# Optimization experiments

Hardware: AMD Instinct MI355X
Metric: run time of the kernel (lower is better)

Reference implementation:

```python
import jax, jax.numpy as jnp
import numpy as np

HUGE = 1e8  # stand-in for ops.HUGE_INT

B, P, Q, PD, QD = 16, 1024, 512, 768, 768


def setup_inputs() -> dict:
    key = jax.random.key(0)
    k1, k2, k3, k4, k5 = jax.random.split(key, 5)
    p = jax.random.normal(k1, (B, P, PD), dtype=jnp.float32)
    q = jax.random.normal(k2, (B, Q, QD), dtype=jnp.float32)
    # True = padded position (masked out before softmax)
    p_masks = jax.random.randint(k3, (B, P), 0, 2).astype(bool)
    q_masks = jax.random.randint(k4, (B, Q), 0, 2).astype(bool)
    # projection weight of Linear(q_dim, p_dim, bias=False): [p_dim, q_dim]
    W = jax.random.normal(k5, (PD, QD), dtype=jnp.float32) / np.sqrt(QD)
    return {"p": p, "q": q, "p_masks": p_masks, "q_masks": q_masks, "W": W}


def reference(p, q, p_masks, q_masks, W):
    # q_proj = project(q): [B,Q,p_dim]; dropout=0.0 -> identity
    q_proj = jnp.einsum('bqd,pd->bqp', q, W)
    # affinity = p @ q_proj^T : [B,P,Q]
    affinity = jnp.einsum('bpd,bqd->bpq', p, q_proj)
    # normalize over dim 1 with padding mask broadcast over last dim
    attn_over_p = jax.nn.softmax(
        jnp.where(p_masks[:, :, None], -HUGE, affinity), axis=1)  # [B,P,Q]
    attn_over_q = jax.nn.softmax(
        jnp.where(q_masks[:, :, None], -HUGE, jnp.swapaxes(affinity, 1, 2)), axis=1)  # [B,Q,P]
    # attn(weights[B,W2,W3], cand[B,W2,C3]) -> [B,W3,C3] = weights^T @ cand
    q_to_p_attn_vec = jnp.einsum('bpq,bpd->bqd', attn_over_p, p)  # [B,Q,p_dim]
    cand = jnp.concatenate([q, q_to_p_attn_vec], axis=2)  # [B,Q,q_dim+p_dim]
    p_to_q_attn_vec = jnp.einsum('bqp,bqc->bpc', attn_over_q, cand)  # [B,P,q_dim+p_dim]
    return (p_to_q_attn_vec, q_to_p_attn_vec)
```

## Files before the change

kernel.cpp:

```cpp
#include <hip/hip_runtime.h>
#include <math.h>

constexpr int B_  = 16;
constexpr int P_  = 1024;
constexpr int Q_  = 512;
constexpr int PD_ = 768;
constexpr int QD_ = 768;
constexpr int CD_ = 1536;

#define HUGE_NEG (-1e8f)

typedef __attribute__((ext_vector_type(8))) _Float16 f16x8;
typedef __attribute__((ext_vector_type(4))) _Float16 f16x4;
typedef __attribute__((ext_vector_type(4))) float f32x4;

__device__ __forceinline__ void dma16(const void* g, void* l) {
  __builtin_amdgcn_global_load_lds((__attribute__((address_space(1))) void*)g,
                                   (__attribute__((address_space(3))) void*)l,
                                   16, 0, 0);
}

__global__ __launch_bounds__(256) void k_cvt(const float* __restrict__ src,
                                             _Float16* __restrict__ dst, int n8) {
  int i = blockIdx.x * 256 + threadIdx.x;
  if (i >= n8) return;
  float4 a = ((const float4*)src)[2 * i];
  float4 b = ((const float4*)src)[2 * i + 1];
  f16x8 o = {(_Float16)a.x, (_Float16)a.y, (_Float16)a.z, (_Float16)a.w,
             (_Float16)b.x, (_Float16)b.y, (_Float16)b.z, (_Float16)b.w};
  ((f16x8*)dst)[i] = o;
}

__global__ __launch_bounds__(256) void k_t2b16(const float* __restrict__ src,
                                               _Float16* __restrict__ dst,
                                               int R, int C, size_t dstBatch,
                                               int colOff) {
  __shared__ _Float16 T[64][72];
  int r0 = blockIdx.x * 64, c0 = blockIdx.y * 64, b = blockIdx.z;
  const float* S = src + (size_t)b * R * C;
  int tid = threadIdx.x;
  int rr = tid >> 4;
  int cc = (tid & 15) * 4;
#pragma unroll
  for (int k = 0; k < 4; ++k) {
    int r = rr + k * 16;
    float4 v = *(const float4*)(S + (size_t)(r0 + r) * C + c0 + cc);
    T[cc + 0][r] = (_Float16)v.x;
    T[cc + 1][r] = (_Float16)v.y;
    T[cc + 2][r] = (_Float16)v.z;
    T[cc + 3][r] = (_Float16)v.w;
  }
  __syncthreads();
  int cr = tid >> 2;
  int rc = (tid & 3) * 16;
  _Float16* D = dst + (size_t)b * dstBatch + (size_t)(colOff + c0 + cr) * R + r0;
  *(f16x8*)(D + rc) = *(f16x8*)&T[cr][rc];
  *(f16x8*)(D + rc + 8) = *(f16x8*)&T[cr][rc + 8];
}

__global__ __launch_bounds__(256) void k_rowWP(const float* __restrict__ aff,
                                               const int* __restrict__ qmask,
                                               _Float16* __restrict__ WP) {
  int row = blockIdx.x * 4 + (threadIdx.x >> 6);
  int lane = threadIdx.x & 63;
  int b = row >> 10;
  const float* r = aff + (size_t)row * Q_;
  const int* qm = qmask + b * Q_;
  int q0 = lane * 4;
  float4 x = *(const float4*)(r + q0);
  float4 y = *(const float4*)(r + q0 + 256);
  int4 ma = *(const int4*)(qm + q0);
  int4 mb = *(const int4*)(qm + q0 + 256);
  float v[8];
  v[0] = ma.x ? HUGE_NEG : x.x;
  v[1] = ma.y ? HUGE_NEG : x.y;
  v[2] = ma.z ? HUGE_NEG : x.z;
  v[3] = ma.w ? HUGE_NEG : x.w;
  v[4] = mb.x ? HUGE_NEG : y.x;
  v[5] = mb.y ? HUGE_NEG : y.y;
  v[6] = mb.z ? HUGE_NEG : y.z;
  v[7] = mb.w ? HUGE_NEG : y.w;
  float m = v[0];
#pragma unroll
  for (int j = 1; j < 8; ++j) m = fmaxf(m, v[j]);
#pragma unroll
  for (int off = 32; off > 0; off >>= 1) m = fmaxf(m, __shfl_xor(m, off));
  float s = 0.f;
#pragma unroll
  for (int j = 0; j < 8; ++j) s += __expf(v[j] - m);
#pragma unroll
  for (int off = 32; off > 0; off >>= 1) s += __shfl_xor(s, off);
  float inv = 1.0f / s;
  f16x4 w0, w1;
#pragma unroll
  for (int j = 0; j < 4; ++j) {
    w0[j] = (_Float16)(__expf(v[j] - m) * inv);
    w1[j] = (_Float16)(__expf(v[j + 4] - m) * inv);
  }
  _Float16* D = WP + (size_t)row * Q_;
  *(f16x4*)(D + q0) = w0;
  *(f16x4*)(D + q0 + 256) = w1;
}

__global__ __launch_bounds__(256) void k_colmerge(
    const float* __restrict__ pmax_part, const float* __restrict__ psum_part,
    float* __restrict__ colmax, float* __restrict__ colsum) {
  int b = blockIdx.x;
  int q = blockIdx.y * 256 + threadIdx.x;
  float m = -INFINITY;
#pragma unroll
  for (int z = 0; z < 8; ++z) m = fmaxf(m, pmax_part[(b * 8 + z) * Q_ + q]);
  float s = 0.f;
#pragma unroll
  for (int z = 0; z < 8; ++z)
    s += psum_part[(b * 8 + z) * Q_ + q] *
         __expf(pmax_part[(b * 8 + z) * Q_ + q] - m);
  colmax[b * Q_ + q] = m;
  colsum[b * Q_ + q] = s;
}

__global__ __launch_bounds__(256) void k_wq16(const float* __restrict__ aff,
                                              const int* __restrict__ pmask,
                                              const float* __restrict__ colmax,
                                              const float* __restrict__ colsum,
                                              _Float16* __restrict__ WQ) {
  __shared__ _Float16 T[64][72];
  __shared__ float cmx[64], cinv[64];
  int p0 = blockIdx.x * 64, q0 = blockIdx.y * 64, b = blockIdx.z;
  int tid = threadIdx.x;
  if (tid < 64) {
    cmx[tid] = colmax[b * Q_ + q0 + tid];
    cinv[tid] = 1.0f / colsum[b * Q_ + q0 + tid];
  }
  __syncthreads();
  const float* A = aff + (size_t)b * P_ * Q_;
  const int* pm = pmask + b * P_;
  int rr = tid >> 4;
  int cc = (tid & 15) * 4;
#pragma unroll
  for (int k = 0; k < 4; ++k) {
    int r = rr + k * 16;
    int msk = pm[p0 + r];
    float4 v = *(const float4*)(A + (size_t)(p0 + r) * Q_ + q0 + cc);
    float vv[4] = {v.x, v.y, v.z, v.w};
#pragma unroll
    for (int j = 0; j < 4; ++j) {
      float e = __expf((msk ? HUGE_NEG : vv[j]) - cmx[cc + j]) * cinv[cc + j];
      T[cc + j][r] = (_Float16)e;
    }
  }
  __syncthreads();
  int cr = tid >> 2;
  int rc = (tid & 3) * 16;
  _Float16* D = WQ + ((size_t)b * Q_ + q0 + cr) * P_ + p0;
  *(f16x8*)(D + rc) = *(f16x8*)&T[cr][rc];
  *(f16x8*)(D + rc + 8) = *(f16x8*)&T[cr][rc + 8];
}

template <int NT, int LDA, int LDB>
__device__ __forceinline__ void gemm_core(const _Float16* __restrict__ Ab,
                                          const _Float16* __restrict__ Bb,
                                          _Float16* As, _Float16* Bs,
                                          f32x4 (&acc)[4][4], int w, int l) {
  constexpr int TSZ = 128 * 32;
  int rA = w * 32 + (l >> 2);
  int sA = ((l & 3) ^ ((rA >> 1) & 3)) * 8;
  int fr = l & 15;
  int fsw = (((l >> 4) ^ ((fr >> 1) & 3))) * 8;
  int wr = w >> 1, wc = w & 1;

  auto stage = [&](int buf, int t) {
    const _Float16* ga = Ab + (size_t)rA * LDA + t * 32 + sA;
    const _Float16* gb = Bb + (size_t)rA * LDB + t * 32 + sA;
    _Float16* la = As + buf * TSZ + (w * 32) * 32;
    _Float16* lb = Bs + buf * TSZ + (w * 32) * 32;
    dma16(ga, la);
    dma16(ga + 16 * LDA, la + 16 * 32);
    dma16(gb, lb);
    dma16(gb + 16 * LDB, lb + 16 * 32);
  };
  auto compute = [&](int buf) {
    const _Float16* A0 = As + buf * TSZ;
    const _Float16* B0 = Bs + buf * TSZ;
    f16x8 a[4];
#pragma unroll
    for (int m = 0; m < 4; ++m)
      a[m] = *(const f16x8*)(A0 + (wr * 64 + m * 16 + fr) * 32 + fsw);
#pragma unroll
    for (int n = 0; n < 4; ++n) {
      f16x8 bn = *(const f16x8*)(B0 + (wc * 64 + n * 16 + fr) * 32 + fsw);
#pragma unroll
      for (int m = 0; m < 4; ++m)
        acc[m][n] =
            __builtin_amdgcn_mfma_f32_16x16x32_f16(a[m], bn, acc[m][n], 0, 0, 0);
    }
  };

  stage(0, 0);
  stage(1, 1);
  int b0 = 0, b1 = 1, b2 = 2;
#pragma unroll 3
  for (int t = 0; t < NT - 2; ++t) {
    stage(b2, t + 2);
    asm volatile("s_waitcnt vmcnt(8)" ::: "memory");
    __builtin_amdgcn_s_barrier();
    __builtin_amdgcn_sched_barrier(0);
    compute(b0);
    __builtin_amdgcn_s_barrier();
    int tmp = b0; b0 = b1; b1 = b2; b2 = tmp;
  }
  asm volatile("s_waitcnt vmcnt(4)" ::: "memory");
  __builtin_amdgcn_s_barrier();
  __builtin_amdgcn_sched_barrier(0);
  compute(b0);
  __builtin_amdgcn_s_barrier();
  asm volatile("s_waitcnt vmcnt(0)" ::: "memory");
  __builtin_amdgcn_s_barrier();
  __builtin_amdgcn_sched_barrier(0);
  compute(b1);
}

#define SWZ_DECODE(GX, GY)                                          \
  int lin = blockIdx.x + (GX) * (blockIdx.y + (GY) * blockIdx.z);   \
  constexpr int NWG = (GX) * (GY) * B_;                             \
  int w8 = (lin & 7) * (NWG / 8) + (lin >> 3);                      \
  int j0 = (w8 % (GX)) * 128;                                      \
  int t_ = w8 / (GX);                                               \
  int i0 = (t_ % (GY)) * 128;                                       \
  int b = t_ / (GY);

__global__ __launch_bounds__(256) void k1_proj(const _Float16* __restrict__ q16,
                                               const _Float16* __restrict__ W16,
                                               _Float16* __restrict__ qp) {
  __shared__ alignas(16) _Float16 As[3 * 128 * 32];
  __shared__ alignas(16) _Float16 Bs[3 * 128 * 32];
  SWZ_DECODE(PD_ / 128, Q_ / 128)
  int tid = threadIdx.x, w = tid >> 6, l = tid & 63;
  f32x4 acc[4][4];
#pragma unroll
  for (int m = 0; m < 4; ++m)
#pragma unroll
    for (int n = 0; n < 4; ++n) acc[m][n] = (f32x4){0.f, 0.f, 0.f, 0.f};
  gemm_core<QD_ / 32, QD_, QD_>(q16 + (size_t)b * Q_ * QD_ + (size_t)i0 * QD_,
                                W16 + (size_t)j0 * QD_, As, Bs, acc, w, l);
  int wr = w >> 1, wc = w & 1, fr = l & 15, fq = l >> 4;
  _Float16* O = qp + (size_t)b * Q_ * PD_;
#pragma unroll
  for (int m = 0; m < 4; ++m) {
    int rl = wr * 64 + m * 16 + fq * 4;
#pragma unroll
    for (int n = 0; n < 4; ++n) {
      int cl = wc * 64 + n * 16 + fr;
#pragma unroll
      for (int r = 0; r < 4; ++r)
        O[(size_t)(i0 + rl + r) * PD_ + j0 + cl] = (_Float16)acc[m][n][r];
    }
  }
}

__global__ __launch_bounds__(256) void k2_aff(const _Float16* __restrict__ p16,
                                              const _Float16* __restrict__ qp,
                                              const int* __restrict__ pmask,
                                              float* __restrict__ aff,
                                              float* __restrict__ pmax_part,
                                              float* __restrict__ psum_part) {
  __shared__ alignas(16) _Float16 As[3 * 128 * 32];
  __shared__ alignas(16) _Float16 Bs[3 * 128 * 32];
  SWZ_DECODE(Q_ / 128, P_ / 128)
  int tid = threadIdx.x, w = tid >> 6, l = tid & 63;
  f32x4 acc[4][4];
#pragma unroll
  for (int m = 0; m < 4; ++m)
#pragma unroll
    for (int n = 0; n < 4; ++n) acc[m][n] = (f32x4){0.f, 0.f, 0.f, 0.f};
  gemm_core<PD_ / 32, PD_, PD_>(p16 + (size_t)b * P_ * PD_ + (size_t)i0 * PD_,
                                qp + (size_t)b * Q_ * PD_ + (size_t)j0 * PD_,
                                As, Bs, acc, w, l);
  int wr = w >> 1, wc = w & 1, fr = l & 15, fq = l >> 4;
  float* Cb = aff + (size_t)b * P_ * Q_;
#pragma unroll
  for (int m = 0; m < 4; ++m) {
    int rl = wr * 64 + m * 16 + fq * 4;
#pragma unroll
    for (int n = 0; n < 4; ++n) {
      int cl = wc * 64 + n * 16 + fr;
#pragma unroll
      for (int r = 0; r < 4; ++r)
        Cb[(size_t)(i0 + rl + r) * Q_ + j0 + cl] = acc[m][n][r];
    }
  }
  const int* pmb = pmask + b * P_ + i0;
  unsigned pmbits = 0;
#pragma unroll
  for (int m = 0; m < 4; ++m)
#pragma unroll
    for (int r = 0; r < 4; ++r)
      pmbits |= (pmb[wr * 64 + m * 16 + fq * 4 + r] ? 1u : 0u) << (m * 4 + r);
  __syncthreads();
  float* redm = (float*)As;
  float* reds = redm + 256;
#pragma unroll
  for (int n = 0; n < 4; ++n) {
    float ml = -1e30f;
#pragma unroll
    for (int m = 0; m < 4; ++m)
#pragma unroll
      for (int r = 0; r < 4; ++r) {
        float v = ((pmbits >> (m * 4 + r)) & 1) ? HUGE_NEG : acc[m][n][r];
        ml = fmaxf(ml, v);
      }
    float sl = 0.f;
#pragma unroll
    for (int m = 0; m < 4; ++m)
#pragma unroll
      for (int r = 0; r < 4; ++r) {
        float v = ((pmbits >> (m * 4 + r)) & 1) ? HUGE_NEG : acc[m][n][r];
        sl += __expf(v - ml);
      }
#pragma unroll
    for (int off = 16; off <= 32; off <<= 1) {
      float om = __shfl_xor(ml, off);
      float os = __shfl_xor(sl, off);
      float nm = fmaxf(ml, om);
      sl = sl * __expf(ml - nm) + os * __expf(om - nm);
      ml = nm;
    }
    if (fq == 0) {
      int col = wc * 64 + n * 16 + fr;
      redm[wr * 128 + col] = ml;
      reds[wr * 128 + col] = sl;
    }
  }
  __syncthreads();
  if (tid < 128) {
    float m0 = redm[tid], m1 = redm[128 + tid];
    float s0 = reds[tid], s1 = reds[128 + tid];
    float nm = fmaxf(m0, m1);
    float ns = s0 * __expf(m0 - nm) + s1 * __expf(m1 - nm);
    int z = i0 >> 7;
    pmax_part[(b * 8 + z) * Q_ + j0 + tid] = nm;
    psum_part[(b * 8 + z) * Q_ + j0 + tid] = ns;
  }
}

__global__ __launch_bounds__(256) void k4_attn(const _Float16* __restrict__ WQ,
                                               const _Float16* __restrict__ pT,
                                               float* __restrict__ out2,
                                               _Float16* __restrict__ candT) {
  __shared__ alignas(16) _Float16 As[3 * 128 * 32];
  __shared__ alignas(16) _Float16 Bs[3 * 128 * 32];
  SWZ_DECODE(PD_ / 128, Q_ / 128)
  int tid = threadIdx.x, w = tid >> 6, l = tid & 63;
  f32x4 acc[4][4];
#pragma unroll
  for (int m = 0; m < 4; ++m)
#pragma unroll
    for (int n = 0; n < 4; ++n) acc[m][n] = (f32x4){0.f, 0.f, 0.f, 0.f};
  gemm_core<P_ / 32, P_, P_>(WQ + (size_t)b * Q_ * P_ + (size_t)i0 * P_,
                             pT + (size_t)b * PD_ * P_ + (size_t)j0 * P_, As,
                             Bs, acc, w, l);
  int wr = w >> 1, wc = w & 1, fr = l & 15, fq = l >> 4;
  float* Cb = out2 + (size_t)b * Q_ * PD_;
  _Float16* Tb = candT + (size_t)b * CD_ * Q_;
#pragma unroll
  for (int m = 0; m < 4; ++m) {
    int rl = wr * 64 + m * 16 + fq * 4;
#pragma unroll
    for (int n = 0; n < 4; ++n) {
      int cl = wc * 64 + n * 16 + fr;
      f16x4 cv;
#pragma unroll
      for (int r = 0; r < 4; ++r) {
        float v = acc[m][n][r];
        Cb[(size_t)(i0 + rl + r) * PD_ + j0 + cl] = v;
        cv[r] = (_Float16)v;
      }
      *(f16x4*)(Tb + (size_t)(QD_ + j0 + cl) * Q_ + i0 + rl) = cv;
    }
  }
}

__global__ __launch_bounds__(256) void k5_attn(const _Float16* __restrict__ WP,
                                               const _Float16* __restrict__ candT,
                                               float* __restrict__ out1) {
  __shared__ alignas(16) _Float16 As[3 * 128 * 32];
  __shared__ alignas(16) _Float16 Bs[3 * 128 * 32];
  SWZ_DECODE(CD_ / 128, P_ / 128)
  int tid = threadIdx.x, w = tid >> 6, l = tid & 63;
  f32x4 acc[4][4];
#pragma unroll
  for (int m = 0; m < 4; ++m)
#pragma unroll
    for (int n = 0; n < 4; ++n) acc[m][n] = (f32x4){0.f, 0.f, 0.f, 0.f};
  gemm_core<Q_ / 32, Q_, Q_>(WP + (size_t)b * P_ * Q_ + (size_t)i0 * Q_,
                             candT + (size_t)b * CD_ * Q_ + (size_t)j0 * Q_, As,
                             Bs, acc, w, l);
  int wr = w >> 1, wc = w & 1, fr = l & 15, fq = l >> 4;
  float* Cb = out1 + (size_t)b * P_ * CD_;
#pragma unroll
  for (int m = 0; m < 4; ++m) {
    int rl = wr * 64 + m * 16 + fq * 4;
#pragma unroll
    for (int n = 0; n < 4; ++n) {
      int cl = wc * 64 + n * 16 + fr;
#pragma unroll
      for (int r = 0; r < 4; ++r)
        Cb[(size_t)(i0 + rl + r) * CD_ + j0 + cl] = acc[m][n][r];
    }
  }
}

extern "C" void kernel_launch(void* const* d_in, const int* in_sizes, int n_in,
                              void* d_out, int out_size, void* d_ws,
                              size_t ws_size, hipStream_t stream) {
  const float* p = (const float*)d_in[0];
  const float* q = (const float*)d_in[1];
  const int* pmask = (const int*)d_in[2];
  const int* qmask = (const int*)d_in[3];
  const float* W = (const float*)d_in[4];
  float* out = (float*)d_out;

  char* ws = (char*)d_ws;
  size_t off = 0;
  auto alloc = [&](size_t bytes) {
    void* r = ws + off;
    off += (bytes + 255) & ~(size_t)255;
    return r;
  };
  _Float16* qh16 = (_Float16*)alloc((size_t)B_ * Q_ * QD_ * 2);
  _Float16* qp16 = (_Float16*)alloc((size_t)B_ * Q_ * PD_ * 2);
  _Float16* candT = qh16;
  _Float16* Wh16 = (_Float16*)alloc((size_t)PD_ * QD_ * 2);
  _Float16* ph16 = (_Float16*)alloc((size_t)B_ * P_ * PD_ * 2);
  _Float16* pT = ph16;
  float* aff = (float*)alloc((size_t)B_ * P_ * Q_ * 4);
  _Float16* WP = (_Float16*)alloc((size_t)B_ * P_ * Q_ * 2);
  _Float16* WQ = (_Float16*)alloc((size_t)B_ * Q_ * P_ * 2);
  float* colmax = (float*)alloc((size_t)B_ * Q_ * 4);
  float* colsum = (float*)alloc((size_t)B_ * Q_ * 4);
  float* pmax_part = (float*)alloc((size_t)B_ * 8 * Q_ * 4);
  float* psum_part = (float*)alloc((size_t)B_ * 8 * Q_ * 4);

  float* out1 = out;
  float* out2 = out + (size_t)B_ * P_ * CD_;

  k_cvt<<<B_ * Q_ * QD_ / 8 / 256, 256, 0, stream>>>(q, qh16, B_ * Q_ * QD_ / 8);
  k_cvt<<<PD_ * QD_ / 8 / 256, 256, 0, stream>>>(W, Wh16, PD_ * QD_ / 8);
  k_cvt<<<B_ * P_ * PD_ / 8 / 256, 256, 0, stream>>>(p, ph16, B_ * P_ * PD_ / 8);
  k1_proj<<<dim3(PD_ / 128, Q_ / 128, B_), 256, 0, stream>>>(qh16, Wh16, qp16);
  k2_aff<<<dim3(Q_ / 128, P_ / 128, B_), 256, 0, stream>>>(
      ph16, qp16, pmask, aff, pmax_part, psum_part);
  k_rowWP<<<B_ * P_ / 4, 256, 0, stream>>>(aff, qmask, WP);
  k_colmerge<<<dim3(B_, Q_ / 256), 256, 0, stream>>>(pmax_part, psum_part,
                                                     colmax, colsum);
  k_wq16<<<dim3(P_ / 64, Q_ / 64, B_), 256, 0, stream>>>(aff, pmask, colmax,
                                                         colsum, WQ);
  k_t2b16<<<dim3(P_ / 64, PD_ / 64, B_), 256, 0, stream>>>(
      p, pT, P_, PD_, (size_t)PD_ * P_, 0);
  k4_attn<<<dim3(PD_ / 128, Q_ / 128, B_), 256, 0, stream>>>(WQ, pT, out2,
                                                             candT);
  k_t2b16<<<dim3(Q_ / 64, QD_ / 64, B_), 256, 0, stream>>>(
      q, candT, Q_, QD_, (size_t)CD_ * Q_, 0);
  k5_attn<<<dim3(CD_ / 128, P_ / 128, B_), 256, 0, stream>>>(WP, candT, out1);
}
```

Measured before the change: 169.2 us.

## Widen GEMM tiles to 128x256, fuse row softmax stats into affinity GEMM, merge prep kernels

All four GEMMs now use 128x256 output tiles with double-width B staging and launch bounds allowing two blocks per CU, which raises reuse per loaded tile. The affinity GEMM epilogue also computes per-row max/sum partials, so the separate row-softmax pass over the affinity matrix is replaced by a small merge kernel plus a combined kernel that writes WP and WQ in one read of aff. The fp16 conversion and transpose of p and q are fused into one prep kernel each, dropping separate cvt passes. The cost is more accumulator registers per thread, a larger LDS footprint and fewer blocks in each GEMM grid.

```diff
diff --git a/kernel.cpp b/kernel.cpp
--- a/kernel.cpp
+++ b/kernel.cpp
@@ -31,13 +31,14 @@
   ((f16x8*)dst)[i] = o;
 }
 
-__global__ __launch_bounds__(256) void k_t2b16(const float* __restrict__ src,
-                                               _Float16* __restrict__ dst,
-                                               int R, int C, size_t dstBatch,
-                                               int colOff) {
+__global__ __launch_bounds__(256) void k_prep(const float* __restrict__ src,
+                                              _Float16* __restrict__ dst16,
+                                              _Float16* __restrict__ dstT,
+                                              int R, int C, size_t tBatch) {
   __shared__ _Float16 T[64][72];
   int r0 = blockIdx.x * 64, c0 = blockIdx.y * 64, b = blockIdx.z;
   const float* S = src + (size_t)b * R * C;
+  _Float16* D16 = dst16 + (size_t)b * R * C;
   int tid = threadIdx.x;
   int rr = tid >> 4;
   int cc = (tid & 15) * 4;
@@ -45,61 +46,31 @@
   for (int k = 0; k < 4; ++k) {
     int r = rr + k * 16;
     float4 v = *(const float4*)(S + (size_t)(r0 + r) * C + c0 + cc);
-    T[cc + 0][r] = (_Float16)v.x;
-    T[cc + 1][r] = (_Float16)v.y;
-    T[cc + 2][r] = (_Float16)v.z;
-    T[cc + 3][r] = (_Float16)v.w;
+    f16x4 h = {(_Float16)v.x, (_Float16)v.y, (_Float16)v.z, (_Float16)v.w};
+    *(f16x4*)(D16 + (size_t)(r0 + r) * C + c0 + cc) = h;
+    T[cc + 0][r] = h[0];
+    T[cc + 1][r] = h[1];
+    T[cc + 2][r] = h[2];
+    T[cc + 3][r] = h[3];
   }
   __syncthreads();
   int cr = tid >> 2;
   int rc = (tid & 3) * 16;
-  _Float16* D = dst + (size_t)b * dstBatch + (size_t)(colOff + c0 + cr) * R + r0;
+  _Float16* D = dstT + (size_t)b * tBatch + (size_t)(c0 + cr) * R + r0;
   *(f16x8*)(D + rc) = *(f16x8*)&T[cr][rc];
   *(f16x8*)(D + rc + 8) = *(f16x8*)&T[cr][rc + 8];
 }
 
-__global__ __launch_bounds__(256) void k_rowWP(const float* __restrict__ aff,
-                                               const int* __restrict__ qmask,
-                                               _Float16* __restrict__ WP) {
-  int row = blockIdx.x * 4 + (threadIdx.x >> 6);
-  int lane = threadIdx.x & 63;
-  int b = row >> 10;
-  const float* r = aff + (size_t)row * Q_;
-  const int* qm = qmask + b * Q_;
-  int q0 = lane * 4;
-  float4 x = *(const float4*)(r + q0);
-  float4 y = *(const float4*)(r + q0 + 256);
-  int4 ma = *(const int4*)(qm + q0);
-  int4 mb = *(const int4*)(qm + q0 + 256);
-  float v[8];
-  v[0] = ma.x ? HUGE_NEG : x.x;
-  v[1] = ma.y ? HUGE_NEG : x.y;
-  v[2] = ma.z ? HUGE_NEG : x.z;
-  v[3] = ma.w ? HUGE_NEG : x.w;
-  v[4] = mb.x ? HUGE_NEG : y.x;
-  v[5] = mb.y ? HUGE_NEG : y.y;
-  v[6] = mb.z ? HUGE_NEG : y.z;
-  v[7] = mb.w ? HUGE_NEG : y.w;
-  float m = v[0];
-#pragma unroll
-  for (int j = 1; j < 8; ++j) m = fmaxf(m, v[j]);
-#pragma unroll
-  for (int off = 32; off > 0; off >>= 1) m = fmaxf(m, __shfl_xor(m, off));
-  float s = 0.f;
-#pragma unroll
-  for (int j = 0; j < 8; ++j) s += __expf(v[j] - m);
-#pragma unroll
-  for (int off = 32; off > 0; off >>= 1) s += __shfl_xor(s, off);
-  float inv = 1.0f / s;
-  f16x4 w0, w1;
-#pragma unroll
-  for (int j = 0; j < 4; ++j) {
-    w0[j] = (_Float16)(__expf(v[j] - m) * inv);
-    w1[j] = (_Float16)(__expf(v[j + 4] - m) * inv);
-  }
-  _Float16* D = WP + (size_t)row * Q_;
-  *(f16x4*)(D + q0) = w0;
-  *(f16x4*)(D + q0 + 256) = w1;
+__global__ __launch_bounds__(256) void k_rowmerge(
+    const float* __restrict__ rpm, const float* __restrict__ rps,
+    float* __restrict__ rowmax, float* __restrict__ rowsum) {
+  int idx = blockIdx.x * 256 + threadIdx.x;
+  int b = idx >> 10, p = idx & 1023;
+  float m0 = rpm[(b * 2 + 0) * P_ + p], m1 = rpm[(b * 2 + 1) * P_ + p];
+  float s0 = rps[(b * 2 + 0) * P_ + p], s1 = rps[(b * 2 + 1) * P_ + p];
+  float nm = fmaxf(m0, m1);
+  rowmax[idx] = nm;
+  rowsum[idx] = s0 * __expf(m0 - nm) + s1 * __expf(m1 - nm);
 }
 
 __global__ __launch_bounds__(256) void k_colmerge(
@@ -119,35 +90,45 @@
   colsum[b * Q_ + q] = s;
 }
 
-__global__ __launch_bounds__(256) void k_wq16(const float* __restrict__ aff,
-                                              const int* __restrict__ pmask,
-                                              const float* __restrict__ colmax,
-                                              const float* __restrict__ colsum,
-                                              _Float16* __restrict__ WQ) {
+__global__ __launch_bounds__(256) void k_w(
+    const float* __restrict__ aff, const int* __restrict__ pmask,
+    const int* __restrict__ qmask, const float* __restrict__ rowmax,
+    const float* __restrict__ rowsum, const float* __restrict__ colmax,
+    const float* __restrict__ colsum, _Float16* __restrict__ WP,
+    _Float16* __restrict__ WQ) {
   __shared__ _Float16 T[64][72];
-  __shared__ float cmx[64], cinv[64];
+  __shared__ float rmx[64], rin[64], cmx[64], cin[64];
   int p0 = blockIdx.x * 64, q0 = blockIdx.y * 64, b = blockIdx.z;
   int tid = threadIdx.x;
   if (tid < 64) {
-    cmx[tid] = colmax[b * Q_ + q0 + tid];
-    cinv[tid] = 1.0f / colsum[b * Q_ + q0 + tid];
+    rmx[tid] = rowmax[b * P_ + p0 + tid];
+    rin[tid] = 1.0f / rowsum[b * P_ + p0 + tid];
+  } else if (tid < 128) {
+    int t = tid - 64;
+    cmx[t] = colmax[b * Q_ + q0 + t];
+    cin[t] = 1.0f / colsum[b * Q_ + q0 + t];
   }
   __syncthreads();
   const float* A = aff + (size_t)b * P_ * Q_;
   const int* pm = pmask + b * P_;
   int rr = tid >> 4;
   int cc = (tid & 15) * 4;
+  int4 qm4 = *(const int4*)(qmask + b * Q_ + q0 + cc);
+  int qm[4] = {qm4.x, qm4.y, qm4.z, qm4.w};
 #pragma unroll
   for (int k = 0; k < 4; ++k) {
     int r = rr + k * 16;
     int msk = pm[p0 + r];
     float4 v = *(const float4*)(A + (size_t)(p0 + r) * Q_ + q0 + cc);
     float vv[4] = {v.x, v.y, v.z, v.w};
+    f16x4 wp;
 #pragma unroll
     for (int j = 0; j < 4; ++j) {
-      float e = __expf((msk ? HUGE_NEG : vv[j]) - cmx[cc + j]) * cinv[cc + j];
-      T[cc + j][r] = (_Float16)e;
-    }
+      wp[j] = (_Float16)(__expf((qm[j] ? HUGE_NEG : vv[j]) - rmx[r]) * rin[r]);
+      T[cc + j][r] =
+          (_Float16)(__expf((msk ? HUGE_NEG : vv[j]) - cmx[cc + j]) * cin[cc + j]);
+    }
+    *(f16x4*)(WP + ((size_t)b * P_ + p0 + r) * Q_ + q0 + cc) = wp;
   }
   __syncthreads();
   int cr = tid >> 2;
@@ -161,34 +142,37 @@
 __device__ __forceinline__ void gemm_core(const _Float16* __restrict__ Ab,
                                           const _Float16* __restrict__ Bb,
                                           _Float16* As, _Float16* Bs,
-                                          f32x4 (&acc)[4][4], int w, int l) {
-  constexpr int TSZ = 128 * 32;
-  int rA = w * 32 + (l >> 2);
-  int sA = ((l & 3) ^ ((rA >> 1) & 3)) * 8;
+                                          f32x4 (&acc)[4][8], int w, int l) {
+  constexpr int ASZ = 128 * 32, BSZ = 256 * 32;
+  int rowA = w * 32 + (l >> 2);
+  int rowB = w * 64 + (l >> 2);
+  int sA = ((l & 3) ^ ((l >> 3) & 3)) * 8;
   int fr = l & 15;
-  int fsw = (((l >> 4) ^ ((fr >> 1) & 3))) * 8;
+  int fsw = ((l >> 4) ^ ((fr >> 1) & 3)) * 8;
   int wr = w >> 1, wc = w & 1;
 
   auto stage = [&](int buf, int t) {
-    const _Float16* ga = Ab + (size_t)rA * LDA + t * 32 + sA;
-    const _Float16* gb = Bb + (size_t)rA * LDB + t * 32 + sA;
-    _Float16* la = As + buf * TSZ + (w * 32) * 32;
-    _Float16* lb = Bs + buf * TSZ + (w * 32) * 32;
+    const _Float16* ga = Ab + (size_t)rowA * LDA + t * 32 + sA;
+    _Float16* la = As + buf * ASZ + (w * 32) * 32;
     dma16(ga, la);
     dma16(ga + 16 * LDA, la + 16 * 32);
+    const _Float16* gb = Bb + (size_t)rowB * LDB + t * 32 + sA;
+    _Float16* lb = Bs + buf * BSZ + (w * 64) * 32;
     dma16(gb, lb);
     dma16(gb + 16 * LDB, lb + 16 * 32);
+    dma16(gb + 32 * LDB, lb + 32 * 32);
+    dma16(gb + 48 * LDB, lb + 48 * 32);
   };
   auto compute = [&](int buf) {
-    const _Float16* A0 = As + buf * TSZ;
-    const _Float16* B0 = Bs + buf * TSZ;
+    const _Float16* A0 = As + buf * ASZ;
+    const _Float16* B0 = Bs + buf * BSZ;
     f16x8 a[4];
 #pragma unroll
     for (int m = 0; m < 4; ++m)
       a[m] = *(const f16x8*)(A0 + (wr * 64 + m * 16 + fr) * 32 + fsw);
 #pragma unroll
-    for (int n = 0; n < 4; ++n) {
-      f16x8 bn = *(const f16x8*)(B0 + (wc * 64 + n * 16 + fr) * 32 + fsw);
+    for (int n = 0; n < 8; ++n) {
+      f16x8 bn = *(const f16x8*)(B0 + (wc * 128 + n * 16 + fr) * 32 + fsw);
 #pragma unroll
       for (int m = 0; m < 4; ++m)
         acc[m][n] =
@@ -202,14 +186,14 @@
 #pragma unroll 3
   for (int t = 0; t < NT - 2; ++t) {
     stage(b2, t + 2);
-    asm volatile("s_waitcnt vmcnt(8)" ::: "memory");
+    asm volatile("s_waitcnt vmcnt(12)" ::: "memory");
     __builtin_amdgcn_s_barrier();
     __builtin_amdgcn_sched_barrier(0);
     compute(b0);
     __builtin_amdgcn_s_barrier();
     int tmp = b0; b0 = b1; b1 = b2; b2 = tmp;
   }
-  asm volatile("s_waitcnt vmcnt(4)" ::: "memory");
+  asm volatile("s_waitcnt vmcnt(6)" ::: "memory");
   __builtin_amdgcn_s_barrier();
   __builtin_amdgcn_sched_barrier(0);
   compute(b0);
@@ -224,23 +208,23 @@
   int lin = blockIdx.x + (GX) * (blockIdx.y + (GY) * blockIdx.z);   \
   constexpr int NWG = (GX) * (GY) * B_;                             \
   int w8 = (lin & 7) * (NWG / 8) + (lin >> 3);                      \
-  int j0 = (w8 % (GX)) * 128;                                      \
+  int j0 = (w8 % (GX)) * 256;                                       \
   int t_ = w8 / (GX);                                               \
   int i0 = (t_ % (GY)) * 128;                                       \
   int b = t_ / (GY);
 
-__global__ __launch_bounds__(256) void k1_proj(const _Float16* __restrict__ q16,
-                                               const _Float16* __restrict__ W16,
-                                               _Float16* __restrict__ qp) {
+__global__ __launch_bounds__(256, 2) void k1_proj(
+    const _Float16* __restrict__ q16, const _Float16* __restrict__ W16,
+    _Float16* __restrict__ qp) {
   __shared__ alignas(16) _Float16 As[3 * 128 * 32];
-  __shared__ alignas(16) _Float16 Bs[3 * 128 * 32];
-  SWZ_DECODE(PD_ / 128, Q_ / 128)
+  __shared__ alignas(16) _Float16 Bs[3 * 256 * 32];
+  SWZ_DECODE(PD_ / 256, Q_ / 128)
   int tid = threadIdx.x, w = tid >> 6, l = tid & 63;
-  f32x4 acc[4][4];
-#pragma unroll
-  for (int m = 0; m < 4; ++m)
-#pragma unroll
-    for (int n = 0; n < 4; ++n) acc[m][n] = (f32x4){0.f, 0.f, 0.f, 0.f};
+  f32x4 acc[4][8];
+#pragma unroll
+  for (int m = 0; m < 4; ++m)
+#pragma unroll
+    for (int n = 0; n < 8; ++n) acc[m][n] = (f32x4){0.f, 0.f, 0.f, 0.f};
   gemm_core<QD_ / 32, QD_, QD_>(q16 + (size_t)b * Q_ * QD_ + (size_t)i0 * QD_,
                                 W16 + (size_t)j0 * QD_, As, Bs, acc, w, l);
   int wr = w >> 1, wc = w & 1, fr = l & 15, fq = l >> 4;
@@ -249,8 +233,8 @@
   for (int m = 0; m < 4; ++m) {
     int rl = wr * 64 + m * 16 + fq * 4;
 #pragma unroll
-    for (int n = 0; n < 4; ++n) {
-      int cl = wc * 64 + n * 16 + fr;
+    for (int n = 0; n < 8; ++n) {
+      int cl = wc * 128 + n * 16 + fr;
 #pragma unroll
       for (int r = 0; r < 4; ++r)
         O[(size_t)(i0 + rl + r) * PD_ + j0 + cl] = (_Float16)acc[m][n][r];
@@ -258,21 +242,21 @@
   }
 }
 
-__global__ __launch_bounds__(256) void k2_aff(const _Float16* __restrict__ p16,
-                                              const _Float16* __restrict__ qp,
-                                              const int* __restrict__ pmask,
-                                              float* __restrict__ aff,
-                                              float* __restrict__ pmax_part,
-                                              float* __restrict__ psum_part) {
+__global__ __launch_bounds__(256, 2) void k2_aff(
+    const _Float16* __restrict__ p16, const _Float16* __restrict__ qp,
+    const int* __restrict__ pmask, const int* __restrict__ qmask,
+    float* __restrict__ aff, float* __restrict__ pmax_part,
+    float* __restrict__ psum_part, float* __restrict__ rpm,
+    float* __restrict__ rps) {
   __shared__ alignas(16) _Float16 As[3 * 128 * 32];
-  __shared__ alignas(16) _Float16 Bs[3 * 128 * 32];
-  SWZ_DECODE(Q_ / 128, P_ / 128)
+  __shared__ alignas(16) _Float16 Bs[3 * 256 * 32];
+  SWZ_DECODE(Q_ / 256, P_ / 128)
   int tid = threadIdx.x, w = tid >> 6, l = tid & 63;
-  f32x4 acc[4][4];
-#pragma unroll
-  for (int m = 0; m < 4; ++m)
-#pragma unroll
-    for (int n = 0; n < 4; ++n) acc[m][n] = (f32x4){0.f, 0.f, 0.f, 0.f};
+  f32x4 acc[4][8];
+#pragma unroll
+  for (int m = 0; m < 4; ++m)
+#pragma unroll
+    for (int n = 0; n < 8; ++n) acc[m][n] = (f32x4){0.f, 0.f, 0.f, 0.f};
   gemm_core<PD_ / 32, PD_, PD_>(p16 + (size_t)b * P_ * PD_ + (size_t)i0 * PD_,
                                 qp + (size_t)b * Q_ * PD_ + (size_t)j0 * PD_,
                                 As, Bs, acc, w, l);
@@ -282,8 +266,8 @@
   for (int m = 0; m < 4; ++m) {
     int rl = wr * 64 + m * 16 + fq * 4;
 #pragma unroll
-    for (int n = 0; n < 4; ++n) {
-      int cl = wc * 64 + n * 16 + fr;
+    for (int n = 0; n < 8; ++n) {
+      int cl = wc * 128 + n * 16 + fr;
 #pragma unroll
       for (int r = 0; r < 4; ++r)
         Cb[(size_t)(i0 + rl + r) * Q_ + j0 + cl] = acc[m][n][r];
@@ -296,11 +280,21 @@
 #pragma unroll
     for (int r = 0; r < 4; ++r)
       pmbits |= (pmb[wr * 64 + m * 16 + fq * 4 + r] ? 1u : 0u) << (m * 4 + r);
+  int qmv[8];
+  {
+    const int* qmb = qmask + b * Q_ + j0 + wc * 128 + fr;
+#pragma unroll
+    for (int n = 0; n < 8; ++n) qmv[n] = qmb[n * 16];
+  }
   __syncthreads();
-  float* redm = (float*)As;
-  float* reds = redm + 256;
-#pragma unroll
-  for (int n = 0; n < 4; ++n) {
+  float* scr = (float*)As;
+  float* cm_ = scr;
+  float* cs_ = scr + 512;
+  float* rm_ = scr + 1024;
+  float* rs_ = scr + 1280;
+
+#pragma unroll
+  for (int n = 0; n < 8; ++n) {
     float ml = -1e30f;
 #pragma unroll
     for (int m = 0; m < 4; ++m)
@@ -326,36 +320,74 @@
       ml = nm;
     }
     if (fq == 0) {
-      int col = wc * 64 + n * 16 + fr;
-      redm[wr * 128 + col] = ml;
-      reds[wr * 128 + col] = sl;
-    }
-  }
+      int col = wc * 128 + n * 16 + fr;
+      cm_[wr * 256 + col] = ml;
+      cs_[wr * 256 + col] = sl;
+    }
+  }
+#pragma unroll
+  for (int m = 0; m < 4; ++m)
+#pragma unroll
+    for (int r = 0; r < 4; ++r) {
+      float ml = -1e30f;
+#pragma unroll
+      for (int n = 0; n < 8; ++n) {
+        float v = qmv[n] ? HUGE_NEG : acc[m][n][r];
+        ml = fmaxf(ml, v);
+      }
+      float sl = 0.f;
+#pragma unroll
+      for (int n = 0; n < 8; ++n) {
+        float v = qmv[n] ? HUGE_NEG : acc[m][n][r];
+        sl += __expf(v - ml);
+      }
+#pragma unroll
+      for (int off = 1; off <= 8; off <<= 1) {
+        float om = __shfl_xor(ml, off);
+        float os = __shfl_xor(sl, off);
+        float nm = fmaxf(ml, om);
+        sl = sl * __expf(ml - nm) + os * __expf(om - nm);
+        ml = nm;
+      }
+      if (fr == 0) {
+        int row = wr * 64 + m * 16 + fq * 4 + r;
+        rm_[wc * 128 + row] = ml;
+        rs_[wc * 128 + row] = sl;
+      }
+    }
   __syncthreads();
-  if (tid < 128) {
-    float m0 = redm[tid], m1 = redm[128 + tid];
-    float s0 = reds[tid], s1 = reds[128 + tid];
+  if (tid < 256) {
+    float m0 = cm_[tid], m1 = cm_[256 + tid];
+    float s0 = cs_[tid], s1 = cs_[256 + tid];
     float nm = fmaxf(m0, m1);
     float ns = s0 * __expf(m0 - nm) + s1 * __expf(m1 - nm);
     int z = i0 >> 7;
     pmax_part[(b * 8 + z) * Q_ + j0 + tid] = nm;
     psum_part[(b * 8 + z) * Q_ + j0 + tid] = ns;
   }
-}
-
-__global__ __launch_bounds__(256) void k4_attn(const _Float16* __restrict__ WQ,
-                                               const _Float16* __restrict__ pT,
-                                               float* __restrict__ out2,
-                                               _Float16* __restrict__ candT) {
+  if (tid < 128) {
+    float m0 = rm_[tid], m1 = rm_[128 + tid];
+    float s0 = rs_[tid], s1 = rs_[128 + tid];
+    float nm = fmaxf(m0, m1);
+    float ns = s0 * __expf(m0 - nm) + s1 * __expf(m1 - nm);
+    int zj = j0 >> 8;
+    rpm[(b * 2 + zj) * P_ + i0 + tid] = nm;
+    rps[(b * 2 + zj) * P_ + i0 + tid] = ns;
+  }
+}
+
+__global__ __launch_bounds__(256, 2) void k4_attn(
+    const _Float16* __restrict__ WQ, const _Float16* __restrict__ pT,
+    float* __restrict__ out2, _Float16* __restrict__ candT) {
   __shared__ alignas(16) _Float16 As[3 * 128 * 32];
-  __shared__ alignas(16) _Float16 Bs[3 * 128 * 32];
-  SWZ_DECODE(PD_ / 128, Q_ / 128)
+  __shared__ alignas(16) _Float16 Bs[3 * 256 * 32];
+  SWZ_DECODE(PD_ / 256, Q_ / 128)
   int tid = threadIdx.x, w = tid >> 6, l = tid & 63;
-  f32x4 acc[4][4];
-#pragma unroll
-  for (int m = 0; m < 4; ++m)
-#pragma unroll
-    for (int n = 0; n < 4; ++n) acc[m][n] = (f32x4){0.f, 0.f, 0.f, 0.f};
+  f32x4 acc[4][8];
+#pragma unroll
+  for (int m = 0; m < 4; ++m)
+#pragma unroll
+    for (int n = 0; n < 8; ++n) acc[m][n] = (f32x4){0.f, 0.f, 0.f, 0.f};
   gemm_core<P_ / 32, P_, P_>(WQ + (size_t)b * Q_ * P_ + (size_t)i0 * P_,
                              pT + (size_t)b * PD_ * P_ + (size_t)j0 * P_, As,
                              Bs, acc, w, l);
@@ -366,8 +398,8 @@
   for (int m = 0; m < 4; ++m) {
     int rl = wr * 64 + m * 16 + fq * 4;
 #pragma unroll
-    for (int n = 0; n < 4; ++n) {
-      int cl = wc * 64 + n * 16 + fr;
+    for (int n = 0; n < 8; ++n) {
+      int cl = wc * 128 + n * 16 + fr;
       f16x4 cv;
 #pragma unroll
       for (int r = 0; r < 4; ++r) {
@@ -380,18 +412,18 @@
   }
 }
 
-__global__ __launch_bounds__(256) void k5_attn(const _Float16* __restrict__ WP,
-                                               const _Float16* __restrict__ candT,
-                                               float* __restrict__ out1) {
+__global__ __launch_bounds__(256, 2) void k5_attn(
+    const _Float16* __restrict__ WP, const _Float16* __restrict__ candT,
+    float* __restrict__ out1) {
   __shared__ alignas(16) _Float16 As[3 * 128 * 32];
-  __shared__ alignas(16) _Float16 Bs[3 * 128 * 32];
-  SWZ_DECODE(CD_ / 128, P_ / 128)
+  __shared__ alignas(16) _Float16 Bs[3 * 256 * 32];
+  SWZ_DECODE(CD_ / 256, P_ / 128)
   int tid = threadIdx.x, w = tid >> 6, l = tid & 63;
-  f32x4 acc[4][4];
-#pragma unroll
-  for (int m = 0; m < 4; ++m)
-#pragma unroll
-    for (int n = 0; n < 4; ++n) acc[m][n] = (f32x4){0.f, 0.f, 0.f, 0.f};
+  f32x4 acc[4][8];
+#pragma unroll
+  for (int m = 0; m < 4; ++m)
+#pragma unroll
+    for (int n = 0; n < 8; ++n) acc[m][n] = (f32x4){0.f, 0.f, 0.f, 0.f};
   gemm_core<Q_ / 32, Q_, Q_>(WP + (size_t)b * P_ * Q_ + (size_t)i0 * Q_,
                              candT + (size_t)b * CD_ * Q_ + (size_t)j0 * Q_, As,
                              Bs, acc, w, l);
@@ -401,8 +433,8 @@
   for (int m = 0; m < 4; ++m) {
     int rl = wr * 64 + m * 16 + fq * 4;
 #pragma unroll
-    for (int n = 0; n < 4; ++n) {
-      int cl = wc * 64 + n * 16 + fr;
+    for (int n = 0; n < 8; ++n) {
+      int cl = wc * 128 + n * 16 + fr;
 #pragma unroll
       for (int r = 0; r < 4; ++r)
         Cb[(size_t)(i0 + rl + r) * CD_ + j0 + cl] = acc[m][n][r];
@@ -427,39 +459,41 @@
     off += (bytes + 255) & ~(size_t)255;
     return r;
   };
-  _Float16* qh16 = (_Float16*)alloc((size_t)B_ * Q_ * QD_ * 2);
+  _Float16* q16 = (_Float16*)alloc((size_t)B_ * Q_ * QD_ * 2);
+  _Float16* p16 = (_Float16*)alloc((size_t)B_ * P_ * PD_ * 2);
+  _Float16* pT = (_Float16*)alloc((size_t)B_ * PD_ * P_ * 2);
+  _Float16* candT = (_Float16*)alloc((size_t)B_ * CD_ * Q_ * 2);
+  _Float16* W16 = (_Float16*)alloc((size_t)PD_ * QD_ * 2);
   _Float16* qp16 = (_Float16*)alloc((size_t)B_ * Q_ * PD_ * 2);
-  _Float16* candT = qh16;
-  _Float16* Wh16 = (_Float16*)alloc((size_t)PD_ * QD_ * 2);
-  _Float16* ph16 = (_Float16*)alloc((size_t)B_ * P_ * PD_ * 2);
-  _Float16* pT = ph16;
   float* aff = (float*)alloc((size_t)B_ * P_ * Q_ * 4);
   _Float16* WP = (_Float16*)alloc((size_t)B_ * P_ * Q_ * 2);
   _Float16* WQ = (_Float16*)alloc((size_t)B_ * Q_ * P_ * 2);
+  float* rowmax = (float*)alloc((size_t)B_ * P_ * 4);
+  float* rowsum = (float*)alloc((size_t)B_ * P_ * 4);
   float* colmax = (float*)alloc((size_t)B_ * Q_ * 4);
   float* colsum = (float*)alloc((size_t)B_ * Q_ * 4);
   float* pmax_part = (float*)alloc((size_t)B_ * 8 * Q_ * 4);
   float* psum_part = (float*)alloc((size_t)B_ * 8 * Q_ * 4);
+  float* rpm = (float*)alloc((size_t)B_ * 2 * P_ * 4);
+  float* rps = (float*)alloc((size_t)B_ * 2 * P_ * 4);
 
   float* out1 = out;
   float* out2 = out + (size_t)B_ * P_ * CD_;
 
-  k_cvt<<<B_ * Q_ * QD_ / 8 / 256, 256, 0, stream>>>(q, qh16, B_ * Q_ * QD_ / 8);
-  k_cvt<<<PD_ * QD_ / 8 / 256, 256, 0, stream>>>(W, Wh16, PD_ * QD_ / 8);
-  k_cvt<<<B_ * P_ * PD_ / 8 / 256, 256, 0, stream>>>(p, ph16, B_ * P_ * PD_ / 8);
-  k1_proj<<<dim3(PD_ / 128, Q_ / 128, B_), 256, 0, stream>>>(qh16, Wh16, qp16);
-  k2_aff<<<dim3(Q_ / 128, P_ / 128, B_), 256, 0, stream>>>(
-      ph16, qp16, pmask, aff, pmax_part, psum_part);
-  k_rowWP<<<B_ * P_ / 4, 256, 0, stream>>>(aff, qmask, WP);
+  k_cvt<<<PD_ * QD_ / 8 / 256, 256, 0, stream>>>(W, W16, PD_ * QD_ / 8);
+  k_prep<<<dim3(Q_ / 64, QD_ / 64, B_), 256, 0, stream>>>(
+      q, q16, candT, Q_, QD_, (size_t)CD_ * Q_);
+  k_prep<<<dim3(P_ / 64, PD_ / 64, B_), 256, 0, stream>>>(
+      p, p16, pT, P_, PD_, (size_t)PD_ * P_);
+  k1_proj<<<dim3(PD_ / 256, Q_ / 128, B_), 256, 0, stream>>>(q16, W16, qp16);
+  k2_aff<<<dim3(Q_ / 256, P_ / 128, B_), 256, 0, stream>>>(
+      p16, qp16, pmask, qmask, aff, pmax_part, psum_part, rpm, rps);
+  k_rowmerge<<<B_ * P_ / 256, 256, 0, stream>>>(rpm, rps, rowmax, rowsum);
   k_colmerge<<<dim3(B_, Q_ / 256), 256, 0, stream>>>(pmax_part, psum_part,
                                                      colmax, colsum);
-  k_wq16<<<dim3(P_ / 64, Q_ / 64, B_), 256, 0, stream>>>(aff, pmask, colmax,
-                                                         colsum, WQ);
-  k_t2b16<<<dim3(P_ / 64, PD_ / 64, B_), 256, 0, stream>>>(
-      p, pT, P_, PD_, (size_t)PD_ * P_, 0);
-  k4_attn<<<dim3(PD_ / 128, Q_ / 128, B_), 256, 0, stream>>>(WQ, pT, out2,
+  k_w<<<dim3(P_ / 64, Q_ / 64, B_), 256, 0, stream>>>(
+      aff, pmask, qmask, rowmax, rowsum, colmax, colsum, WP, WQ);
+  k4_attn<<<dim3(PD_ / 256, Q_ / 128, B_), 256, 0, stream>>>(WQ, pT, out2,
                                                              candT);
-  k_t2b16<<<dim3(Q_ / 64, QD_ / 64, B_), 256, 0, stream>>>(
-      q, candT, Q_, QD_, (size_t)CD_ * Q_, 0);
-  k5_attn<<<dim3(CD_ / 128, P_ / 128, B_), 256, 0, stream>>>(WP, candT, out1);
-}
+  k5_attn<<<dim3(CD_ / 256, P_ / 128, B_), 256, 0, stream>>>(WP, candT, out1);
+}
```

Measured after the change: 192.8 us. 14.0% more time.
